# Optimization experiments

Hardware: AMD Instinct MI355X
Metric: run time of the kernel (lower is better)

Reference implementation:

```python
import jax, jax.numpy as jnp
import numpy as np

V_TH = 1.0

def setup_inputs() -> dict:
    key = jax.random.key(0)
    x_seq = jax.random.normal(key, (64, 128, 4096), dtype=jnp.float32)
    return {"x_seq": x_seq}

def reference(x_seq):
    # Integrate-and-fire scan over time (axis 0):
    #   v = v + x[t]; s = (v >= v_th); v = v - s * v_th
    v0 = jnp.zeros(x_seq.shape[1:], dtype=x_seq.dtype)

    def step(v, x_t):
        v = v + x_t
        s = (v >= V_TH).astype(x_seq.dtype)
        v = v - s * V_TH
        return v, s

    _, s_seq = jax.lax.scan(step, v0, x_seq)
    return s_seq
```

## Files before the change

### kernel.cpp

```cpp
#include <hip/hip_runtime.h>


#define TSTEPS 64
#define NCOLS (128 * 4096)
#define NCOLS4 (NCOLS / 4)

__global__ __launch_bounds__(256) void TandemIF_86096914416163_kernel(
    const float4* __restrict__ x, float4* __restrict__ out)
{
    const int c = blockIdx.x * 256 + threadIdx.x;
    const float4* xp  = x   + c;
    float4*       op  = out + c;

    float vx = 0.0f, vy = 0.0f, vz = 0.0f, vw = 0.0f;

#pragma unroll 8
    for (int t = 0; t < TSTEPS; ++t) {
        float4 xt = xp[t * NCOLS4];
        vx += xt.x; vy += xt.y; vz += xt.z; vw += xt.w;
        float sx = (vx >= 1.0f) ? 1.0f : 0.0f;
        float sy = (vy >= 1.0f) ? 1.0f : 0.0f;
        float sz = (vz >= 1.0f) ? 1.0f : 0.0f;
        float sw = (vw >= 1.0f) ? 1.0f : 0.0f;
        vx -= sx; vy -= sy; vz -= sz; vw -= sw;
        op[t * NCOLS4] = make_float4(sx, sy, sz, sw);
    }
}

extern "C" void kernel_launch(void* const* d_in, const int* in_sizes, int n_in,
                              void* d_out, int out_size, void* d_ws, size_t ws_size,
                              hipStream_t stream)
{
    const float4* x  = (const float4*)d_in[0];
    float4* out      = (float4*)d_out;
    TandemIF_86096914416163_kernel<<<dim3(NCOLS4 / 256), dim3(256), 0, stream>>>(x, out);
}
```

Baseline: 230.6 us.

## Use float2 per thread, double-buffered batch prefetch, and nontemporal stores

```diff
diff --git a/kernel.cpp b/kernel.cpp
--- a/kernel.cpp
+++ b/kernel.cpp
@@ -1,29 +1,49 @@
 #include <hip/hip_runtime.h>
+#include <string.h>
 
 
 #define TSTEPS 64
-#define NCOLS (128 * 4096)
-#define NCOLS4 (NCOLS / 4)
+#define NCOLS  (128 * 4096)
+#define NCOLS2 (NCOLS / 2)
+#define BATCH  8
 
 __global__ __launch_bounds__(256) void TandemIF_86096914416163_kernel(
-    const float4* __restrict__ x, float4* __restrict__ out)
+    const float2* __restrict__ x, float2* __restrict__ out)
 {
     const int c = blockIdx.x * 256 + threadIdx.x;
-    const float4* xp  = x   + c;
-    float4*       op  = out + c;
+    const float2* xp = x   + c;
+    float2*       op = out + c;
 
-    float vx = 0.0f, vy = 0.0f, vz = 0.0f, vw = 0.0f;
+    float vx = 0.0f, vy = 0.0f;
+    float2 buf[2][BATCH];
 
-#pragma unroll 8
-    for (int t = 0; t < TSTEPS; ++t) {
-        float4 xt = xp[t * NCOLS4];
-        vx += xt.x; vy += xt.y; vz += xt.z; vw += xt.w;
-        float sx = (vx >= 1.0f) ? 1.0f : 0.0f;
-        float sy = (vy >= 1.0f) ? 1.0f : 0.0f;
-        float sz = (vz >= 1.0f) ? 1.0f : 0.0f;
-        float sw = (vw >= 1.0f) ? 1.0f : 0.0f;
-        vx -= sx; vy -= sy; vz -= sz; vw -= sw;
-        op[t * NCOLS4] = make_float4(sx, sy, sz, sw);
+#pragma unroll
+    for (int j = 0; j < BATCH; ++j)
+        buf[0][j] = xp[j * NCOLS2];
+
+#pragma unroll
+    for (int tb = 0; tb < TSTEPS / BATCH; ++tb) {
+        const int cur = tb & 1, nxt = cur ^ 1;
+
+        if (tb < TSTEPS / BATCH - 1) {
+#pragma unroll
+            for (int j = 0; j < BATCH; ++j)
+                buf[nxt][j] = xp[((tb + 1) * BATCH + j) * NCOLS2];
+        }
+
+#pragma unroll
+        for (int j = 0; j < BATCH; ++j) {
+            const float2 xt = buf[cur][j];
+            vx += xt.x; vy += xt.y;
+            const float sx = (vx >= 1.0f) ? 1.0f : 0.0f;
+            const float sy = (vy >= 1.0f) ? 1.0f : 0.0f;
+            vx -= sx; vy -= sy;
+            float2 s = make_float2(sx, sy);
+            double sbits;
+            memcpy(&sbits, &s, sizeof(sbits));
+            __builtin_nontemporal_store(
+                sbits, reinterpret_cast<double*>(op + (tb * BATCH + j) * NCOLS2));
+        }
     }
 }
 
@@ -31,7 +51,7 @@
                               void* d_out, int out_size, void* d_ws, size_t ws_size,
                               hipStream_t stream)
 {
-    const float4* x  = (const float4*)d_in[0];
-    float4* out      = (float4*)d_out;
-    TandemIF_86096914416163_kernel<<<dim3(NCOLS4 / 256), dim3(256), 0, stream>>>(x, out);
+    const float2* x = (const float2*)d_in[0];
+    float2* out     = (float2*)d_out;
+    TandemIF_86096914416163_kernel<<<dim3(NCOLS2 / 256), dim3(256), 0, stream>>>(x, out);
 }
```

Result: faster. 224.6 us (-2.6%).

## Hand-schedule IF scan in inline asm with double-buffered deep load pipelining

Applied to the files above, without the earlier changes.

```diff
diff --git a/kernel.cpp b/kernel.cpp
--- a/kernel.cpp
+++ b/kernel.cpp
@@ -2,36 +2,126 @@
 
 
 #define TSTEPS 64
-#define NCOLS (128 * 4096)
+#define NCOLS  (128 * 4096)
 #define NCOLS4 (NCOLS / 4)
 
+#define LD1(Q)                                                        \
+    "global_load_dwordx4 v[" Q "], v12, %[bx]\n\t"                    \
+    "v_add_u32 v12, 0x200000, v12\n\t"
+
+#define LOAD8_A                                                       \
+    LD1("32:35") LD1("36:39") LD1("40:43") LD1("44:47")               \
+    LD1("48:51") LD1("52:55") LD1("56:59") LD1("60:63")
+
+#define LOAD8_B                                                       \
+    LD1("64:67") LD1("68:71") LD1("72:75") LD1("76:79")               \
+    LD1("80:83") LD1("84:87") LD1("88:91") LD1("92:95")
+
+#define STEP(dx,dy,dz,dw, sx,sy,sz,sw, SQ)                            \
+    "v_add_f32 v8, v8, v" dx "\n\t"                                   \
+    "v_add_f32 v9, v9, v" dy "\n\t"                                   \
+    "v_add_f32 v10, v10, v" dz "\n\t"                                 \
+    "v_add_f32 v11, v11, v" dw "\n\t"                                 \
+    "v_cmp_ge_f32 vcc, v8, v14\n\t"                                   \
+    "v_cndmask_b32 v" sx ", 0, v14, vcc\n\t"                          \
+    "v_cmp_ge_f32 vcc, v9, v14\n\t"                                   \
+    "v_cndmask_b32 v" sy ", 0, v14, vcc\n\t"                          \
+    "v_cmp_ge_f32 vcc, v10, v14\n\t"                                  \
+    "v_cndmask_b32 v" sz ", 0, v14, vcc\n\t"                          \
+    "v_cmp_ge_f32 vcc, v11, v14\n\t"                                  \
+    "v_cndmask_b32 v" sw ", 0, v14, vcc\n\t"                          \
+    "v_sub_f32 v8, v8, v" sx "\n\t"                                   \
+    "v_sub_f32 v9, v9, v" sy "\n\t"                                   \
+    "v_sub_f32 v10, v10, v" sz "\n\t"                                 \
+    "v_sub_f32 v11, v11, v" sw "\n\t"                                 \
+    "global_store_dwordx4 v13, v[" SQ "], %[bo]\n\t"                  \
+    "v_add_u32 v13, 0x200000, v13\n\t"
+
+#define CONSUME_A_SA                                                  \
+    STEP("32","33","34","35",  "96","97","98","99",    "96:99")       \
+    STEP("36","37","38","39",  "100","101","102","103","100:103")     \
+    STEP("40","41","42","43",  "104","105","106","107","104:107")     \
+    STEP("44","45","46","47",  "108","109","110","111","108:111")     \
+    STEP("48","49","50","51",  "112","113","114","115","112:115")     \
+    STEP("52","53","54","55",  "116","117","118","119","116:119")     \
+    STEP("56","57","58","59",  "120","121","122","123","120:123")     \
+    STEP("60","61","62","63",  "124","125","126","127","124:127")
+
+#define CONSUME_B_SB                                                  \
+    STEP("64","65","66","67",  "128","129","130","131","128:131")     \
+    STEP("68","69","70","71",  "132","133","134","135","132:135")     \
+    STEP("72","73","74","75",  "136","137","138","139","136:139")     \
+    STEP("76","77","78","79",  "140","141","142","143","140:143")     \
+    STEP("80","81","82","83",  "144","145","146","147","144:147")     \
+    STEP("84","85","86","87",  "148","149","150","151","148:151")     \
+    STEP("88","89","90","91",  "152","153","154","155","152:155")     \
+    STEP("92","93","94","95",  "156","157","158","159","156:159")
+
 __global__ __launch_bounds__(256) void TandemIF_86096914416163_kernel(
-    const float4* __restrict__ x, float4* __restrict__ out)
+    const float* __restrict__ x, float* __restrict__ out)
 {
     const int c = blockIdx.x * 256 + threadIdx.x;
-    const float4* xp  = x   + c;
-    float4*       op  = out + c;
+    const unsigned voff = (unsigned)c * 16u;
 
-    float vx = 0.0f, vy = 0.0f, vz = 0.0f, vw = 0.0f;
-
-#pragma unroll 8
-    for (int t = 0; t < TSTEPS; ++t) {
-        float4 xt = xp[t * NCOLS4];
-        vx += xt.x; vy += xt.y; vz += xt.z; vw += xt.w;
-        float sx = (vx >= 1.0f) ? 1.0f : 0.0f;
-        float sy = (vy >= 1.0f) ? 1.0f : 0.0f;
-        float sz = (vz >= 1.0f) ? 1.0f : 0.0f;
-        float sw = (vw >= 1.0f) ? 1.0f : 0.0f;
-        vx -= sx; vy -= sy; vz -= sz; vw -= sw;
-        op[t * NCOLS4] = make_float4(sx, sy, sz, sw);
-    }
+    asm volatile(
+        "v_mov_b32 v8, 0\n\t"
+        "v_mov_b32 v9, 0\n\t"
+        "v_mov_b32 v10, 0\n\t"
+        "v_mov_b32 v11, 0\n\t"
+        "v_mov_b32 v14, 1.0\n\t"
+        "v_mov_b32 v12, %[voff]\n\t"
+        "v_mov_b32 v13, %[voff]\n\t"
+        LOAD8_A
+        LOAD8_B
+        "s_waitcnt vmcnt(8)\n\t"
+        CONSUME_A_SA
+        LOAD8_A
+        "s_waitcnt vmcnt(16)\n\t"
+        CONSUME_B_SB
+        LOAD8_B
+        "s_waitcnt vmcnt(16)\n\t"
+        CONSUME_A_SA
+        LOAD8_A
+        "s_waitcnt vmcnt(16)\n\t"
+        CONSUME_B_SB
+        LOAD8_B
+        "s_waitcnt vmcnt(16)\n\t"
+        CONSUME_A_SA
+        LOAD8_A
+        "s_waitcnt vmcnt(16)\n\t"
+        CONSUME_B_SB
+        LOAD8_B
+        "s_waitcnt vmcnt(16)\n\t"
+        CONSUME_A_SA
+        "s_waitcnt vmcnt(8)\n\t"
+        CONSUME_B_SB
+        :
+        : [voff] "v"(voff), [bx] "s"(x), [bo] "s"(out)
+        : "memory", "vcc",
+          "v8","v9","v10","v11","v12","v13","v14",
+          "v32","v33","v34","v35","v36","v37","v38","v39",
+          "v40","v41","v42","v43","v44","v45","v46","v47",
+          "v48","v49","v50","v51","v52","v53","v54","v55",
+          "v56","v57","v58","v59","v60","v61","v62","v63",
+          "v64","v65","v66","v67","v68","v69","v70","v71",
+          "v72","v73","v74","v75","v76","v77","v78","v79",
+          "v80","v81","v82","v83","v84","v85","v86","v87",
+          "v88","v89","v90","v91","v92","v93","v94","v95",
+          "v96","v97","v98","v99","v100","v101","v102","v103",
+          "v104","v105","v106","v107","v108","v109","v110","v111",
+          "v112","v113","v114","v115","v116","v117","v118","v119",
+          "v120","v121","v122","v123","v124","v125","v126","v127",
+          "v128","v129","v130","v131","v132","v133","v134","v135",
+          "v136","v137","v138","v139","v140","v141","v142","v143",
+          "v144","v145","v146","v147","v148","v149","v150","v151",
+          "v152","v153","v154","v155","v156","v157","v158","v159");
 }
 
 extern "C" void kernel_launch(void* const* d_in, const int* in_sizes, int n_in,
                               void* d_out, int out_size, void* d_ws, size_t ws_size,
                               hipStream_t stream)
 {
-    const float4* x  = (const float4*)d_in[0];
-    float4* out      = (float4*)d_out;
+    const float* x = (const float*)d_in[0];
+    float* out     = (float*)d_out;
     TandemIF_86096914416163_kernel<<<dim3(NCOLS4 / 256), dim3(256), 0, stream>>>(x, out);
 }
```

Measured after the change: 228.1 us. Within noise of the previous version (-1.1%).
